# Optimization experiments

Measured on AMD Instinct MI355X. Metric: run time of the kernel, lower is better.

Reference implementation:

```python
import jax, jax.numpy as jnp
import numpy as np

SHIFT, REDUCE = 3, 2
B, L, E, H = 64, 512, 300, 256


def _make_transitions():
    # Left-branching valid parse: S S R S R S R ... (L shifts, L-1 reduces)
    T = 2 * L - 1
    tr = np.full(T, REDUCE, dtype=np.int64)
    tr[0] = SHIFT
    tr[1::2] = SHIFT
    return jnp.asarray(np.tile(tr[None, :], (B, 1)))


def setup_inputs() -> dict:
    key = jax.random.key(0)
    ks = jax.random.split(key, 5)
    s = 0.05
    return {
        "sentence": jax.random.normal(ks[0], (B, L, E), jnp.float32),
        "transitions": _make_transitions(),
        "W_word": jax.random.normal(ks[1], (E, 2 * H), jnp.float32) * s,
        "b_word": jnp.zeros((2 * H,), jnp.float32),
        "W_left": jax.random.normal(ks[2], (H, 5 * H), jnp.float32) * s,
        "W_right": jax.random.normal(ks[3], (H, 5 * H), jnp.float32) * s,
        "b_reduce": jnp.zeros((5 * H,), jnp.float32),
    }


def reference(sentence, transitions, W_word, b_word, W_left, W_right, b_reduce):
    Bsz, Ls, _ = sentence.shape
    Hs = W_left.shape[0]
    proj = sentence @ W_word + b_word                  # [B, L, 2H] (word projection; BN/dropout disabled)
    h_buf, c_buf = jnp.split(proj, 2, axis=2)          # buffers, each [B, L, H]
    T = transitions.shape[1]
    bidx = jnp.arange(Bsz)

    def step(carry, trans_t):
        sh, sc, ptr, bp = carry                        # thin stacks [B,T+2,H], pointers [B]
        shift = trans_t == SHIFT
        i1 = jnp.maximum(ptr - 1, 0)                   # right child (stack top)
        i2 = jnp.maximum(ptr - 2, 0)                   # left child
        hl, cl = sh[bidx, i2], sc[bidx, i2]
        hr, cr = sh[bidx, i1], sc[bidx, i1]
        g = hl @ W_left + hr @ W_right + b_reduce      # [B, 5H] TreeLSTM gates
        ig, flg, frg, og, ug = jnp.split(g, 5, axis=1)
        c_red = (jax.nn.sigmoid(flg) * cl + jax.nn.sigmoid(frg) * cr
                 + jax.nn.sigmoid(ig) * jnp.tanh(ug))
        h_red = jax.nn.sigmoid(og) * jnp.tanh(c_red)
        bsafe = jnp.minimum(bp, Ls - 1)
        val_h = jnp.where(shift[:, None], h_buf[bidx, bsafe], h_red)
        val_c = jnp.where(shift[:, None], c_buf[bidx, bsafe], c_red)
        pos = jnp.where(shift, ptr, i2)                # shift pushes at ptr; reduce writes at ptr-2
        sh = sh.at[bidx, pos].set(val_h)
        sc = sc.at[bidx, pos].set(val_c)
        ptr = ptr + jnp.where(shift, 1, -1)
        bp = bp + shift.astype(bp.dtype)
        return (sh, sc, ptr, bp), None

    sh0 = jnp.zeros((Bsz, T + 2, Hs), sentence.dtype)
    sc0 = jnp.zeros((Bsz, T + 2, Hs), sentence.dtype)
    ptr0 = jnp.zeros((Bsz,), jnp.int32)
    bp0 = jnp.zeros((Bsz,), jnp.int32)
    (sh, sc, ptr, _), _ = jax.lax.scan(
        step, (sh0, sc0, ptr0, bp0), jnp.swapaxes(transitions, 0, 1))
    return sh[bidx, jnp.maximum(ptr - 1, 0)]           # final stack top h: [B, H]
```

## Files before the change

### kernel.cpp

```cpp
#include <hip/hip_runtime.h>
#include <hip/hip_bf16.h>
#include <math.h>

#define BSZ   64
#define LSEQ  512
#define EDIM  300
#define HDIM  256
#define TLEN  1023
#define PROJW 512
#define GW    1280

#define NROW  8
#define NHID  8
#define NBLK  256
#define SLOTS 2
#define DMAX  512

#define PROJ_N   (BSZ*LSEQ*PROJW)
#define STACKF   PROJ_N
#define PAIRB    (STACKF/2)
#define PAIR_CNT (2*BSZ*SLOTS*HDIM)

#define TSENT   0xFFFFu
#define SENT    0xFFFFFFFFu
#define NODEBIT 0x80000000u
#define LROW    264
#define HRO     (NROW*LROW + 4)
#define RPITCH  328
#define RROW    41

__global__ void __launch_bounds__(256)
proj_gemm(const float* __restrict__ A, const float* __restrict__ W,
          const float* __restrict__ bias, float* __restrict__ out) {
    __shared__ float As[8][65];
    __shared__ float Bs[8][64];
    const int tid = threadIdx.x;
    const int tx = tid & 15, ty = tid >> 4;
    const int bm = blockIdx.y, bn = blockIdx.x;

    float acc[4][4] = {};
    const int e  = tid * 2;
    const int ar = e >> 3, ac = e & 7;
    const int br = e >> 6, bc = e & 63;

    for (int k0 = 0; k0 < EDIM; k0 += 8) {
        __syncthreads();
        {
            const float* Ap = A + (size_t)(bm * 64 + ar) * EDIM;
            int gk = k0 + ac;
            As[ac][ar]     = (gk     < EDIM) ? Ap[gk]     : 0.f;
            As[ac + 1][ar] = (gk + 1 < EDIM) ? Ap[gk + 1] : 0.f;
            int gkb = k0 + br;
            float w0 = 0.f, w1 = 0.f;
            if (gkb < EDIM) {
                const float* Wp = W + (size_t)gkb * PROJW + bn * 64;
                w0 = Wp[bc]; w1 = Wp[bc + 1];
            }
            Bs[br][bc] = w0; Bs[br][bc + 1] = w1;
        }
        __syncthreads();
        #pragma unroll
        for (int kk = 0; kk < 8; ++kk) {
            float a[4], b[4];
            #pragma unroll
            for (int i = 0; i < 4; ++i) a[i] = As[kk][ty * 4 + i];
            #pragma unroll
            for (int j = 0; j < 4; ++j) b[j] = Bs[kk][tx * 4 + j];
            #pragma unroll
            for (int i = 0; i < 4; ++i)
                #pragma unroll
                for (int j = 0; j < 4; ++j)
                    acc[i][j] += a[i] * b[j];
        }
    }
    #pragma unroll
    for (int i = 0; i < 4; ++i) {
        const int row  = bm * 64 + ty * 4 + i;
        const int col0 = bn * 64 + tx * 4;
        float* op = out + (size_t)row * PROJW + col0;
        #pragma unroll
        for (int j = 0; j < 4; ++j) op[j] = acc[i][j] + bias[col0 + j];
    }
}

__device__ __forceinline__ int qswz(int Q, int row) {
    return Q ^ row ^ ((Q >> 3) & 7);
}
__device__ __forceinline__ unsigned long long pld(const unsigned long long* p) {
    return __hip_atomic_load(p, __ATOMIC_RELAXED, __HIP_MEMORY_SCOPE_AGENT);
}
__device__ __forceinline__ void fetch_octet(const unsigned long long* pb,
                                            unsigned ee, float* h) {
    for (;;) {
        unsigned long long v[8];
        #pragma unroll
        for (int i = 0; i < 8; ++i) v[i] = pld(pb + i);
        bool ok = true;
        #pragma unroll
        for (int i = 0; i < 8; ++i) ok &= ((unsigned)(v[i] >> 32) >= ee);
        if (ok) {
            #pragma unroll
            for (int i = 0; i < 8; ++i) h[i] = __uint_as_float((unsigned)v[i]);
            return;
        }
        __builtin_amdgcn_s_sleep(1);
    }
}

__global__ void __launch_bounds__(256, 1)
scan_coop(const int* __restrict__ trans,
          const float* __restrict__ Wl, const float* __restrict__ Wr,
          const float* __restrict__ bred,
          float* __restrict__ ws, float* __restrict__ out) {
    __shared__ __align__(16) float hbuf[HRO + NROW * LROW];
    __shared__ __align__(16) float red[16 * RPITCH];
    __shared__ float    cstk[4 * NROW * NHID];
    __shared__ unsigned tbits[NROW][32];
    __shared__ unsigned fbits[32];
    __shared__ unsigned desc[DMAX][NROW][3];
    __shared__ unsigned d_oh[NROW], e_oh[NROW];

    const int tid   = threadIdx.x;
    const int rg    = blockIdx.x & 7;
    const int cs    = blockIdx.x >> 3;
    const int rbase = rg * NROW;
    const int n0    = cs * NHID;

    const int srow = tid >> 5, sc = tid & 31;
    const int colq = tid & 7;
    const int rh   = (tid >> 3) & 1;
    const int m    = (tid >> 4) & 1;
    const int w8   = tid >> 5;
    const int gn   = n0 + colq;
    const int wv   = tid >> 6;
    const int lane = tid & 63;
    const bool fin = (lane < 16);
    const int frow = 2 * wv + (lane >> 3);
    const int fcol = lane & 7;
    const int fgn  = n0 + fcol;

    unsigned long long* p64 = (unsigned long long*)ws;

    float4 w[8][5];
    {
        const float* src = (m == 0) ? Wl : Wr;
        const int kbase = w8 * 32;
        #pragma unroll
        for (int j = 0; j < 8; ++j) {
            const int k0 = kbase + j * 4;
            #pragma unroll
            for (int g = 0; g < 5; ++g) {
                w[j][g].x = src[(size_t)(k0 + 0) * GW + g * HDIM + gn];
                w[j][g].y = src[(size_t)(k0 + 1) * GW + g * HDIM + gn];
                w[j][g].z = src[(size_t)(k0 + 2) * GW + g * HDIM + gn];
                w[j][g].w = src[(size_t)(k0 + 3) * GW + g * HDIM + gn];
            }
        }
    }
    #pragma unroll
    for (int j = 0; j < 8; ++j)
        #pragma unroll
        for (int g = 0; g < 5; ++g)
            asm volatile("" : "+v"(w[j][g].x), "+v"(w[j][g].y),
                              "+v"(w[j][g].z), "+v"(w[j][g].w));

    if (tid < NROW * 32) {
        const int r2 = tid >> 5, wd = tid & 31;
        unsigned bits = 0;
        for (int j = 0; j < 32; ++j) {
            const int t = wd * 32 + j;
            if (t < TLEN && trans[(size_t)(rbase + r2) * TLEN + t] == 3) bits |= (1u << j);
        }
        tbits[r2][wd] = bits;
    }
    __syncthreads();
    if (tid < 32) {
        unsigned fb = 0;
        #pragma unroll
        for (int r2 = 0; r2 < NROW; ++r2) fb |= ~tbits[r2][tid];
        if (tid == 31) fb &= 0x7FFFFFFFu;
        fbits[tid] = fb;
    }
    __syncthreads();
    unsigned EPOCHS = 0;
    for (int i = 0; i < 32; ++i) EPOCHS += (unsigned)__popc(fbits[i]);
    if (EPOCHS > DMAX - 1) EPOCHS = DMAX - 1;

    if (tid < NROW) {
        const int r = tid, grow = rbase + r;
        int ptr = 0, bp = 0;
        unsigned tg0 = TSENT, tg1 = TSENT;
        unsigned ep0 = 0, ep1 = 0;
        unsigned n = 0;
        for (int t = 0; t < TLEN; ++t) {
            const int redstep = (fbits[t >> 5] >> (t & 31)) & 1;
            if (redstep) ++n;
            const int is_shift = (tbits[r][t >> 5] >> (t & 31)) & 1;
            if (is_shift) {
                const int pos = max(0, min(ptr, SLOTS - 1));
                const unsigned wt = (unsigned)min(bp, LSEQ - 1);
                if (pos == 0) tg0 = wt; else tg1 = wt;
                ptr++; bp++;
                if (redstep && n < DMAX) desc[n][r][2] = 0;
            } else {
                const int i1 = min(max(ptr - 1, 0), SLOTS - 1);
                const int i2 = min(max(ptr - 2, 0), SLOTS - 1);
                const unsigned t1 = i1 ? tg1 : tg0;
                const unsigned t2 = i2 ? tg1 : tg0;
                const unsigned e1 = i1 ? ep1 : ep0;
                const unsigned e2 = i2 ? ep1 : ep0;
                const int t2node = (t2 != TSENT) && (t2 & 0x8000u);
                const int pnew = (t2node && !((t2 >> 1) & 1)) ? 1 : 0;
                if (n < DMAX) {
                    desc[n][r][0] = t2 | (t1 << 16);
                    desc[n][r][1] = e2 | (e1 << 16);
                    desc[n][r][2] = 1u | ((unsigned)(pnew * 2 + i2) << 1);
                }
                const unsigned newtag = 0x8000u | ((unsigned)pnew << 1) | (unsigned)i2;
                if (i2 == 0) { tg0 = newtag; ep0 = n; }
                else         { tg1 = newtag; ep1 = n; }
                ptr--;
            }
        }
        const int top = min(max(ptr - 1, 0), SLOTS - 1);
        const unsigned tt = top ? tg1 : tg0;
        const unsigned te = top ? ep1 : ep0;
        if (tt == TSENT) { d_oh[r] = SENT; e_oh[r] = 0; }
        else if (!(tt & 0x8000u)) {
            d_oh[r] = (unsigned)((grow * LSEQ + (int)tt) * PROJW); e_oh[r] = 0;
        } else {
            d_oh[r] = NODEBIT | (unsigned)(PAIRB +
                      ((((tt >> 1) & 1) * BSZ + grow) * SLOTS + (tt & 1)) * HDIM);
            e_oh[r] = te;
        }
    }
    __syncthreads();

    float bv[5];
    #pragma unroll
    for (int g = 0; g < 5; ++g) bv[g] = bred[g * HDIM + gn];

    auto stage = [&](unsigned e) {
        const unsigned dsc2 = desc[e][srow][2];
        if (!(dsc2 & 1)) return;
        const unsigned dsc0 = desc[e][srow][0];
        const unsigned dsc1 = desc[e][srow][1];
        const unsigned tagL = dsc0 & 0xFFFFu, tagR = dsc0 >> 16;
        const unsigned eeL = dsc1 & 0xFFFFu, eeR = dsc1 >> 16;
        const int grow = rbase + srow;
        const bool ndL = (tagL != TSENT) && (tagL & 0x8000u);
        const bool ndR = (tagR != TSENT) && (tagR & 0x8000u);
        float h0[8], h1[8];

        if (tagL == TSENT) {
            #pragma unroll
            for (int i = 0; i < 8; ++i) h0[i] = 0.f;
        } else if (!ndL) {
            const float* p = ws + (size_t)(grow * LSEQ + (int)tagL) * PROJW + sc * 8;
            const float4 a = *(const float4*)p;
            const float4 b = *(const float4*)(p + 4);
            h0[0]=a.x; h0[1]=a.y; h0[2]=a.z; h0[3]=a.w;
            h0[4]=b.x; h0[5]=b.y; h0[6]=b.z; h0[7]=b.w;
        }
        if (tagR == TSENT) {
            #pragma unroll
            for (int i = 0; i < 8; ++i) h1[i] = 0.f;
        } else if (!ndR) {
            const float* p = ws + (size_t)(grow * LSEQ + (int)tagR) * PROJW + sc * 8;
            const float4 a = *(const float4*)p;
            const float4 b = *(const float4*)(p + 4);
            h1[0]=a.x; h1[1]=a.y; h1[2]=a.z; h1[3]=a.w;
            h1[4]=b.x; h1[5]=b.y; h1[6]=b.z; h1[7]=b.w;
        }
        if (ndL)
            fetch_octet(p64 + PAIRB +
                ((((tagL >> 1) & 1) * BSZ + grow) * SLOTS + (tagL & 1)) * HDIM + sc * 8,
                eeL, h0);
        if (ndR)
            fetch_octet(p64 + PAIRB +
                ((((tagR >> 1) & 1) * BSZ + grow) * SLOTS + (tagR & 1)) * HDIM + sc * 8,
                eeR, h1);

        *(float4*)&hbuf[srow * LROW + 4 * qswz(2 * sc + 0, srow)] =
            make_float4(h0[0], h0[1], h0[2], h0[3]);
        *(float4*)&hbuf[srow * LROW + 4 * qswz(2 * sc + 1, srow)] =
            make_float4(h0[4], h0[5], h0[6], h0[7]);
        *(float4*)&hbuf[HRO + srow * LROW + 4 * qswz(2 * sc + 0, srow)] =
            make_float4(h1[0], h1[1], h1[2], h1[3]);
        *(float4*)&hbuf[HRO + srow * LROW + 4 * qswz(2 * sc + 1, srow)] =
            make_float4(h1[4], h1[5], h1[6], h1[7]);
    };

    if (EPOCHS >= 1) stage(1);

    for (unsigned e = 1; e <= EPOCHS; ++e) {
        __syncthreads();

        float clw = 0.f, crw = 0.f;
        unsigned fd2 = 0, ftagL = TSENT, ftagR = TSENT;
        if (fin) {
            fd2 = desc[e][frow][2];
            if (fd2 & 1) {
                const unsigned d0 = desc[e][frow][0];
                ftagL = d0 & 0xFFFFu; ftagR = d0 >> 16;
                const int fg = rbase + frow;
                if (ftagL != TSENT && !(ftagL & 0x8000u))
                    clw = ws[(size_t)(fg * LSEQ + (int)ftagL) * PROJW + HDIM + fgn];
                if (ftagR != TSENT && !(ftagR & 0x8000u))
                    crw = ws[(size_t)(fg * LSEQ + (int)ftagR) * PROJW + HDIM + fgn];
            }
        }

        float acc[4][5];
        #pragma unroll
        for (int r = 0; r < 4; ++r)
            #pragma unroll
            for (int g = 0; g < 5; ++g) acc[r][g] = 0.f;
        {
            const float* hb = hbuf + m * HRO;
            #pragma unroll
            for (int j = 0; j < 8; ++j) {
                const int kq = w8 * 8 + j;
                #pragma unroll
                for (int r = 0; r < 4; ++r) {
                    const int row = rh * 4 + r;
                    const float4 x = *(const float4*)&hb[row * LROW + 4 * qswz(kq, row)];
                    #pragma unroll
                    for (int g = 0; g < 5; ++g)
                        acc[r][g] += x.x * w[j][g].x + x.y * w[j][g].y
                                   + x.z * w[j][g].z + x.w * w[j][g].w;
                }
            }
        }
        {
            const int g16 = w8 * 2 + m;
            #pragma unroll
            for (int r = 0; r < 4; ++r) {
                const int row = rh * 4 + r;
                #pragma unroll
                for (int g = 0; g < 5; ++g)
                    red[g16 * RPITCH + row * RROW + colq * 5 + g] = acc[r][g];
            }
        }
        __syncthreads();

        if (fin && (fd2 & 1)) {
            float s[5];
            #pragma unroll
            for (int g = 0; g < 5; ++g) s[g] = bv[g];
            #pragma unroll
            for (int q = 0; q < 16; ++q)
                #pragma unroll
                for (int g = 0; g < 5; ++g)
                    s[g] += red[q * RPITCH + frow * RROW + fcol * 5 + g];
            float cl;
            if (ftagL == TSENT) cl = 0.f;
            else if (ftagL & 0x8000u) cl = cstk[((ftagL & 3u) * NROW + frow) * NHID + fcol];
            else cl = clw;
            float cr;
            if (ftagR == TSENT) cr = 0.f;
            else if (ftagR & 0x8000u) cr = cstk[((ftagR & 3u) * NROW + frow) * NHID + fcol];
            else cr = crw;
            const float si = 1.f / (1.f + expf(-s[0]));
            const float sl = 1.f / (1.f + expf(-s[1]));
            const float sr = 1.f / (1.f + expf(-s[2]));
            const float so = 1.f / (1.f + expf(-s[3]));
            const float c_red = sl * cl + sr * cr + si * tanhf(s[4]);
            const float h_red = so * tanhf(c_red);
            const unsigned cw = (fd2 >> 1) & 3u;
            cstk[(cw * NROW + frow) * NHID + fcol] = c_red;
            const unsigned dwr = (unsigned)(PAIRB +
                (((cw >> 1) * BSZ + (rbase + frow)) * SLOTS + (cw & 1)) * HDIM);
            const unsigned long long pv =
                ((unsigned long long)e << 32) | (unsigned long long)__float_as_uint(h_red);
            __hip_atomic_store(p64 + dwr + fgn, pv,
                               __ATOMIC_RELAXED, __HIP_MEMORY_SCOPE_AGENT);
        }
        if (e < EPOCHS) stage(e + 1);
    }

    __syncthreads();

    if (tid < 64) {
        const int orow = tid >> 3;
        const int ocol = n0 + (tid & 7);
        const unsigned oh = d_oh[orow];
        float v;
        if (oh == SENT) v = 0.f;
        else if (!(oh & NODEBIT)) v = ws[oh + ocol];
        else {
            const unsigned long long* pb = p64 + (oh & ~NODEBIT) + ocol;
            const unsigned ee = e_oh[orow];
            unsigned long long pv;
            for (;;) {
                pv = pld(pb);
                if ((unsigned)(pv >> 32) >= ee) break;
                __builtin_amdgcn_s_sleep(1);
            }
            v = __uint_as_float((unsigned)pv);
        }
        out[(size_t)(rbase + orow) * HDIM + ocol] = v;
    }
}

extern "C" void kernel_launch(void* const* d_in, const int* in_sizes, int n_in,
                              void* d_out, int out_size, void* d_ws, size_t ws_size,
                              hipStream_t stream) {
    const float* sentence    = (const float*)d_in[0];
    const int*   transitions = (const int*)  d_in[1];
    const float* W_word      = (const float*)d_in[2];
    const float* b_word      = (const float*)d_in[3];
    const float* W_left      = (const float*)d_in[4];
    const float* W_right     = (const float*)d_in[5];
    const float* b_reduce    = (const float*)d_in[6];
    float* out  = (float*)d_out;
    float* ws_f = (float*)d_ws;

    hipMemsetAsync((char*)d_ws + (size_t)STACKF * 4, 0,
                   (size_t)PAIR_CNT * 8, stream);

    dim3 g1(PROJW / 64, (BSZ * LSEQ) / 64);
    proj_gemm<<<g1, 256, 0, stream>>>(sentence, W_word, b_word, ws_f);

    scan_coop<<<NBLK, 256, 0, stream>>>(transitions, W_left, W_right, b_reduce,
                                        ws_f, out);
}
```

Before: 2.900 ms.

## Precompute right-child word GEMM for next epoch off the critical dependency path

```diff
diff --git a/kernel.cpp b/kernel.cpp
--- a/kernel.cpp
+++ b/kernel.cpp
@@ -25,7 +25,9 @@
 #define SENT    0xFFFFFFFFu
 #define NODEBIT 0x80000000u
 #define LROW    264
-#define HRO     (NROW*LROW + 4)
+#define HLSZ    (NROW*LROW)
+#define HRB0    (HLSZ + 4)
+#define HRSZ    (HLSZ + 4)
 #define RPITCH  328
 #define RROW    41
 
@@ -112,7 +114,7 @@
           const float* __restrict__ Wl, const float* __restrict__ Wr,
           const float* __restrict__ bred,
           float* __restrict__ ws, float* __restrict__ out) {
-    __shared__ __align__(16) float hbuf[HRO + NROW * LROW];
+    __shared__ __align__(16) float hbuf[HRB0 + 2 * HRSZ];
     __shared__ __align__(16) float red[16 * RPITCH];
     __shared__ float    cstk[4 * NROW * NHID];
     __shared__ unsigned tbits[NROW][32];
@@ -129,8 +131,7 @@
     const int srow = tid >> 5, sc = tid & 31;
     const int colq = tid & 7;
     const int rh   = (tid >> 3) & 1;
-    const int m    = (tid >> 4) & 1;
-    const int w8   = tid >> 5;
+    const int ksl  = tid >> 4;
     const int gn   = n0 + colq;
     const int wv   = tid >> 6;
     const int lane = tid & 63;
@@ -141,28 +142,33 @@
 
     unsigned long long* p64 = (unsigned long long*)ws;
 
-    float4 w[8][5];
+    float4 wl[4][5], wr[4][5];
     {
-        const float* src = (m == 0) ? Wl : Wr;
-        const int kbase = w8 * 32;
-        #pragma unroll
-        for (int j = 0; j < 8; ++j) {
-            const int k0 = kbase + j * 4;
+        #pragma unroll
+        for (int j = 0; j < 4; ++j) {
+            const int k0 = ksl * 16 + j * 4;
             #pragma unroll
             for (int g = 0; g < 5; ++g) {
-                w[j][g].x = src[(size_t)(k0 + 0) * GW + g * HDIM + gn];
-                w[j][g].y = src[(size_t)(k0 + 1) * GW + g * HDIM + gn];
-                w[j][g].z = src[(size_t)(k0 + 2) * GW + g * HDIM + gn];
-                w[j][g].w = src[(size_t)(k0 + 3) * GW + g * HDIM + gn];
+                wl[j][g].x = Wl[(size_t)(k0 + 0) * GW + g * HDIM + gn];
+                wl[j][g].y = Wl[(size_t)(k0 + 1) * GW + g * HDIM + gn];
+                wl[j][g].z = Wl[(size_t)(k0 + 2) * GW + g * HDIM + gn];
+                wl[j][g].w = Wl[(size_t)(k0 + 3) * GW + g * HDIM + gn];
+                wr[j][g].x = Wr[(size_t)(k0 + 0) * GW + g * HDIM + gn];
+                wr[j][g].y = Wr[(size_t)(k0 + 1) * GW + g * HDIM + gn];
+                wr[j][g].z = Wr[(size_t)(k0 + 2) * GW + g * HDIM + gn];
+                wr[j][g].w = Wr[(size_t)(k0 + 3) * GW + g * HDIM + gn];
             }
         }
     }
     #pragma unroll
-    for (int j = 0; j < 8; ++j)
-        #pragma unroll
-        for (int g = 0; g < 5; ++g)
-            asm volatile("" : "+v"(w[j][g].x), "+v"(w[j][g].y),
-                              "+v"(w[j][g].z), "+v"(w[j][g].w));
+    for (int j = 0; j < 4; ++j)
+        #pragma unroll
+        for (int g = 0; g < 5; ++g) {
+            asm volatile("" : "+v"(wl[j][g].x), "+v"(wl[j][g].y),
+                              "+v"(wl[j][g].z), "+v"(wl[j][g].w));
+            asm volatile("" : "+v"(wr[j][g].x), "+v"(wr[j][g].y),
+                              "+v"(wr[j][g].z), "+v"(wr[j][g].w));
+        }
 
     if (tid < NROW * 32) {
         const int r2 = tid >> 5, wd = tid & 31;
@@ -240,58 +246,105 @@
     #pragma unroll
     for (int g = 0; g < 5; ++g) bv[g] = bred[g * HDIM + gn];
 
-    auto stage = [&](unsigned e) {
+    auto stage_hl = [&](unsigned e) {
         const unsigned dsc2 = desc[e][srow][2];
         if (!(dsc2 & 1)) return;
-        const unsigned dsc0 = desc[e][srow][0];
-        const unsigned dsc1 = desc[e][srow][1];
-        const unsigned tagL = dsc0 & 0xFFFFu, tagR = dsc0 >> 16;
-        const unsigned eeL = dsc1 & 0xFFFFu, eeR = dsc1 >> 16;
+        const unsigned tagL = desc[e][srow][0] & 0xFFFFu;
+        const unsigned eeL  = desc[e][srow][1] & 0xFFFFu;
         const int grow = rbase + srow;
-        const bool ndL = (tagL != TSENT) && (tagL & 0x8000u);
-        const bool ndR = (tagR != TSENT) && (tagR & 0x8000u);
-        float h0[8], h1[8];
-
+        float h0[8];
         if (tagL == TSENT) {
             #pragma unroll
             for (int i = 0; i < 8; ++i) h0[i] = 0.f;
-        } else if (!ndL) {
+        } else if (!(tagL & 0x8000u)) {
             const float* p = ws + (size_t)(grow * LSEQ + (int)tagL) * PROJW + sc * 8;
             const float4 a = *(const float4*)p;
             const float4 b = *(const float4*)(p + 4);
             h0[0]=a.x; h0[1]=a.y; h0[2]=a.z; h0[3]=a.w;
             h0[4]=b.x; h0[5]=b.y; h0[6]=b.z; h0[7]=b.w;
-        }
+        } else {
+            fetch_octet(p64 + PAIRB +
+                ((((tagL >> 1) & 1) * BSZ + grow) * SLOTS + (tagL & 1)) * HDIM + sc * 8,
+                eeL, h0);
+        }
+        *(float4*)&hbuf[srow * LROW + 4 * qswz(2 * sc + 0, srow)] =
+            make_float4(h0[0], h0[1], h0[2], h0[3]);
+        *(float4*)&hbuf[srow * LROW + 4 * qswz(2 * sc + 1, srow)] =
+            make_float4(h0[4], h0[5], h0[6], h0[7]);
+    };
+    auto stage_hr_words = [&](unsigned e) {
+        const unsigned dsc2 = desc[e][srow][2];
+        if (!(dsc2 & 1)) return;
+        const unsigned tagR = desc[e][srow][0] >> 16;
+        const int grow = rbase + srow;
+        float* hb = hbuf + HRB0 + (e & 1) * HRSZ;
+        float h1[8];
         if (tagR == TSENT) {
             #pragma unroll
             for (int i = 0; i < 8; ++i) h1[i] = 0.f;
-        } else if (!ndR) {
+        } else if (!(tagR & 0x8000u)) {
             const float* p = ws + (size_t)(grow * LSEQ + (int)tagR) * PROJW + sc * 8;
             const float4 a = *(const float4*)p;
             const float4 b = *(const float4*)(p + 4);
             h1[0]=a.x; h1[1]=a.y; h1[2]=a.z; h1[3]=a.w;
             h1[4]=b.x; h1[5]=b.y; h1[6]=b.z; h1[7]=b.w;
-        }
-        if (ndL)
-            fetch_octet(p64 + PAIRB +
-                ((((tagL >> 1) & 1) * BSZ + grow) * SLOTS + (tagL & 1)) * HDIM + sc * 8,
-                eeL, h0);
-        if (ndR)
-            fetch_octet(p64 + PAIRB +
-                ((((tagR >> 1) & 1) * BSZ + grow) * SLOTS + (tagR & 1)) * HDIM + sc * 8,
-                eeR, h1);
-
-        *(float4*)&hbuf[srow * LROW + 4 * qswz(2 * sc + 0, srow)] =
-            make_float4(h0[0], h0[1], h0[2], h0[3]);
-        *(float4*)&hbuf[srow * LROW + 4 * qswz(2 * sc + 1, srow)] =
-            make_float4(h0[4], h0[5], h0[6], h0[7]);
-        *(float4*)&hbuf[HRO + srow * LROW + 4 * qswz(2 * sc + 0, srow)] =
+        } else return;
+        *(float4*)&hb[srow * LROW + 4 * qswz(2 * sc + 0, srow)] =
             make_float4(h1[0], h1[1], h1[2], h1[3]);
-        *(float4*)&hbuf[HRO + srow * LROW + 4 * qswz(2 * sc + 1, srow)] =
+        *(float4*)&hb[srow * LROW + 4 * qswz(2 * sc + 1, srow)] =
             make_float4(h1[4], h1[5], h1[6], h1[7]);
     };
-
-    if (EPOCHS >= 1) stage(1);
+    auto stage_hr_nodes = [&](unsigned e) {
+        const unsigned dsc2 = desc[e][srow][2];
+        if (!(dsc2 & 1)) return;
+        const unsigned tagR = desc[e][srow][0] >> 16;
+        if (tagR == TSENT || !(tagR & 0x8000u)) return;
+        const unsigned eeR = desc[e][srow][1] >> 16;
+        const int grow = rbase + srow;
+        float* hb = hbuf + HRB0 + (e & 1) * HRSZ;
+        float h1[8];
+        fetch_octet(p64 + PAIRB +
+            ((((tagR >> 1) & 1) * BSZ + grow) * SLOTS + (tagR & 1)) * HDIM + sc * 8,
+            eeR, h1);
+        *(float4*)&hb[srow * LROW + 4 * qswz(2 * sc + 0, srow)] =
+            make_float4(h1[0], h1[1], h1[2], h1[3]);
+        *(float4*)&hb[srow * LROW + 4 * qswz(2 * sc + 1, srow)] =
+            make_float4(h1[4], h1[5], h1[6], h1[7]);
+    };
+
+    float acc[4][5];
+    auto gemmR = [&](unsigned ee) {
+        #pragma unroll
+        for (int r = 0; r < 4; ++r)
+            #pragma unroll
+            for (int g = 0; g < 5; ++g) acc[r][g] = 0.f;
+        const float* hb = hbuf + HRB0 + (ee & 1) * HRSZ;
+        unsigned tagR4[4];
+        #pragma unroll
+        for (int r = 0; r < 4; ++r) tagR4[r] = desc[ee][rh * 4 + r][0] >> 16;
+        #pragma unroll
+        for (int j = 0; j < 4; ++j) {
+            const int kq = ksl * 4 + j;
+            #pragma unroll
+            for (int r = 0; r < 4; ++r) {
+                const int row = rh * 4 + r;
+                if (tagR4[r] != TSENT && (tagR4[r] & 0x8000u)) continue;
+                const float4 x = *(const float4*)&hb[row * LROW + 4 * qswz(kq, row)];
+                #pragma unroll
+                for (int g = 0; g < 5; ++g)
+                    acc[r][g] += x.x * wr[j][g].x + x.y * wr[j][g].y
+                               + x.z * wr[j][g].z + x.w * wr[j][g].w;
+            }
+        }
+    };
+
+    if (EPOCHS >= 1) {
+        stage_hr_words(1);
+        stage_hl(1);
+        stage_hr_nodes(1);
+    }
+    __syncthreads();
+    if (EPOCHS >= 1) gemmR(1);
 
     for (unsigned e = 1; e <= EPOCHS; ++e) {
         __syncthreads();
@@ -311,37 +364,49 @@
             }
         }
 
-        float acc[4][5];
-        #pragma unroll
-        for (int r = 0; r < 4; ++r)
-            #pragma unroll
-            for (int g = 0; g < 5; ++g) acc[r][g] = 0.f;
         {
-            const float* hb = hbuf + m * HRO;
-            #pragma unroll
-            for (int j = 0; j < 8; ++j) {
-                const int kq = w8 * 8 + j;
+            const float* hb = hbuf;
+            #pragma unroll
+            for (int j = 0; j < 4; ++j) {
+                const int kq = ksl * 4 + j;
                 #pragma unroll
                 for (int r = 0; r < 4; ++r) {
                     const int row = rh * 4 + r;
                     const float4 x = *(const float4*)&hb[row * LROW + 4 * qswz(kq, row)];
                     #pragma unroll
                     for (int g = 0; g < 5; ++g)
-                        acc[r][g] += x.x * w[j][g].x + x.y * w[j][g].y
-                                   + x.z * w[j][g].z + x.w * w[j][g].w;
+                        acc[r][g] += x.x * wl[j][g].x + x.y * wl[j][g].y
+                                   + x.z * wl[j][g].z + x.w * wl[j][g].w;
                 }
             }
+            #pragma unroll
+            for (int r = 0; r < 4; ++r) {
+                const int row = rh * 4 + r;
+                const unsigned tagR = desc[e][row][0] >> 16;
+                if ((desc[e][row][2] & 1) && tagR != TSENT && (tagR & 0x8000u)) {
+                    const float* hr2 = hbuf + HRB0 + (e & 1) * HRSZ;
+                    #pragma unroll
+                    for (int j = 0; j < 4; ++j) {
+                        const int kq = ksl * 4 + j;
+                        const float4 x = *(const float4*)&hr2[row * LROW + 4 * qswz(kq, row)];
+                        #pragma unroll
+                        for (int g = 0; g < 5; ++g)
+                            acc[r][g] += x.x * wr[j][g].x + x.y * wr[j][g].y
+                                       + x.z * wr[j][g].z + x.w * wr[j][g].w;
+                    }
+                }
+            }
         }
         {
-            const int g16 = w8 * 2 + m;
             #pragma unroll
             for (int r = 0; r < 4; ++r) {
                 const int row = rh * 4 + r;
                 #pragma unroll
                 for (int g = 0; g < 5; ++g)
-                    red[g16 * RPITCH + row * RROW + colq * 5 + g] = acc[r][g];
-            }
-        }
+                    red[ksl * RPITCH + row * RROW + colq * 5 + g] = acc[r][g];
+            }
+        }
+        if (e < EPOCHS) stage_hr_words(e + 1);
         __syncthreads();
 
         if (fin && (fd2 & 1)) {
@@ -376,7 +441,11 @@
             __hip_atomic_store(p64 + dwr + fgn, pv,
                                __ATOMIC_RELAXED, __HIP_MEMORY_SCOPE_AGENT);
         }
-        if (e < EPOCHS) stage(e + 1);
+        if (e < EPOCHS) {
+            gemmR(e + 1);
+            stage_hl(e + 1);
+            stage_hr_nodes(e + 1);
+        }
     }
 
     __syncthreads();
```

Result: slower. 3.062 ms (+5.6%).
